# Kernel tuning notes

Hardware: AMD Instinct MI355X
Metric: run time of the kernel (lower is better)

The kernel has to match this reference:

```python
import jax, jax.numpy as jnp
import numpy as np

EPS = 1e-5  # torch BatchNorm default eps
SLOPE = 0.2  # LeakyReLU negative slope


def bn_apply(h, p):
    # p: (4, C) stacked [gamma, beta, running_mean, running_var]; h channel-last
    g, b, m, v = p[0], p[1], p[2], p[3]
    return (h - m) * (g * jax.lax.rsqrt(v + EPS)) + b


def graph_feature(x, k):
    # x: (B, N, C) -> (B, N, k, 2C) = concat(neighbor - center, center)
    inner = jnp.einsum('bnc,bmc->bnm', x, x)
    sq = jnp.sum(x * x, axis=-1)
    # negative squared pairwise distance (B, N, N)
    pd = 2.0 * inner - sq[:, :, None] - sq[:, None, :]
    idx = jax.lax.top_k(pd, k)[1]  # (B, N, k)
    nbr = jax.vmap(lambda xb, ib: xb[ib])(x, idx)  # (B, N, k, C) gather
    ctr = jnp.broadcast_to(x[:, :, None, :], nbr.shape)
    return jnp.concatenate([nbr - ctr, ctr], axis=-1)


def edge_block(h, w, bnp, k):
    # h: (B, N, C); w: (O, 2C) 1x1 conv weight; returns (B, N, O) after max over k
    f = graph_feature(h, k)
    z = jnp.einsum('bnkc,oc->bnko', f, w)
    z = jax.nn.leaky_relu(bn_apply(z, bnp), SLOPE)
    return jnp.max(z, axis=2)


def setup_inputs() -> dict:
    key = jax.random.key(0)
    ks = jax.random.split(key, 10)
    B, N, K = 16, 1024, 20
    emb, ncls = 1024, 40

    def bnp(c):
        return jnp.stack([jnp.ones(c), jnp.zeros(c), jnp.zeros(c), jnp.ones(c)])

    s = 0.05
    return {
        'x': jax.random.normal(ks[0], (B, 3, N), dtype=jnp.float32),
        'w1': jax.random.normal(ks[1], (64, 6), dtype=jnp.float32) * s,
        'bn1': bnp(64),
        'w2': jax.random.normal(ks[2], (64, 128), dtype=jnp.float32) * s,
        'bn2': bnp(64),
        'w3': jax.random.normal(ks[3], (128, 128), dtype=jnp.float32) * s,
        'bn3': bnp(128),
        'w4': jax.random.normal(ks[4], (256, 256), dtype=jnp.float32) * s,
        'bn4': bnp(256),
        'w5': jax.random.normal(ks[5], (emb, 512), dtype=jnp.float32) * s,
        'bn5': bnp(emb),
        'wl1': jax.random.normal(ks[6], (512, 2 * emb), dtype=jnp.float32) * s,
        'bn6': bnp(512),
        'wl2': jax.random.normal(ks[7], (256, 512), dtype=jnp.float32) * s,
        'bn7': bnp(256),
        'wl3': jax.random.normal(ks[8], (ncls, 256), dtype=jnp.float32) * s,
        'bl3': jax.random.normal(ks[9], (ncls,), dtype=jnp.float32) * s,
        'k': K,
    }


def reference(x, w1, bn1, w2, bn2, w3, bn3, w4, bn4, w5, bn5,
              wl1, bn6, wl2, bn7, wl3, bl3, k):
    # x: (B, 3, N) -> logits (B, num_classes); eval-mode BN, dropout = identity
    h0 = jnp.transpose(x, (0, 2, 1))  # (B, N, 3)
    x1 = edge_block(h0, w1, bn1, k)   # (B, N, 64)
    x2 = edge_block(x1, w2, bn2, k)   # (B, N, 64)
    x3 = edge_block(x2, w3, bn3, k)   # (B, N, 128)
    x4 = edge_block(x3, w4, bn4, k)   # (B, N, 256)
    h = jnp.concatenate([x1, x2, x3, x4], axis=-1)  # (B, N, 512)
    h = jax.nn.leaky_relu(bn_apply(jnp.einsum('bnc,oc->bno', h, w5), bn5), SLOPE)
    p = jnp.concatenate([jnp.max(h, axis=1), jnp.mean(h, axis=1)], axis=-1)  # (B, 2*emb)
    h = jax.nn.leaky_relu(bn_apply(p @ wl1.T, bn6), SLOPE)
    h = jax.nn.leaky_relu(bn_apply(h @ wl2.T, bn7), SLOPE)
    return h @ wl3.T + bl3
```

## Files before the change

kernel.cpp:

```cpp
#include <hip/hip_runtime.h>

#define BB 16
#define NN 1024
#define KNN 20
#define BNEPS 1e-5f

typedef __attribute__((ext_vector_type(8))) short short8;
typedef __attribute__((ext_vector_type(4))) float f32x4;

__device__ __forceinline__ float4 ld4(const float* p){ return *(const float4*)p; }
__device__ __forceinline__ void fma4(float4& a, float s, float4 w){
  a.x = fmaf(s, w.x, a.x); a.y = fmaf(s, w.y, a.y);
  a.z = fmaf(s, w.z, a.z); a.w = fmaf(s, w.w, a.w);
}
__device__ __forceinline__ void max4(float4& a, float4 v){
  a.x = fmaxf(a.x, v.x); a.y = fmaxf(a.y, v.y);
  a.z = fmaxf(a.z, v.z); a.w = fmaxf(a.w, v.w);
}
__device__ __forceinline__ unsigned short f2bf(float f){
  unsigned int u = __float_as_uint(f);
  u = (u + 0x7FFF + ((u >> 16) & 1)) >> 16;
  return (unsigned short)u;
}
__device__ __forceinline__ float bf2f(unsigned short u){
  return __uint_as_float(((unsigned int)u) << 16);
}
__device__ __forceinline__ f32x4 mfma16(short8 a, short8 b, f32x4 c){
  return __builtin_amdgcn_mfma_f32_16x16x32_bf16(a, b, c, 0, 0, 0);
}

__device__ __forceinline__ void top3_build(const float* rp, int kmr,
                                           float& a0, float& a1, float& a2,
                                           int& i0, int& i1, int& i2){
  a0 = -1e30f; a1 = -1e30f; a2 = -1e30f; i0 = 0; i1 = 0; i2 = 0;
#pragma unroll
  for (int r = 0; r < 4; r++){
    float4 t = ld4(rp + r*4);
    float tv[4] = {t.x, t.y, t.z, t.w};
#pragma unroll
    for (int q = 0; q < 4; q++){
      int e = r*4 + q;
      float v = ((kmr >> e) & 1) ? -1e30f : tv[q];
      bool b0 = v > a0, b1 = v > a1, b2 = v > a2;
      a2 = b1 ? a1 : (b2 ? v : a2); i2 = b1 ? i1 : (b2 ? e : i2);
      a1 = b0 ? a0 : (b1 ? v : a1); i1 = b0 ? i0 : (b1 ? e : i1);
      a0 = b0 ? v  : a0;            i0 = b0 ? e : i0;
    }
  }
}

__global__ __launch_bounds__(256) void k_transpose(const float* __restrict__ x, float* __restrict__ xt,
                                                   unsigned short* __restrict__ hlo,
                                                   float* __restrict__ sq){
  int i = blockIdx.x*256 + threadIdx.x;
  if (i >= BB*NN) return;
  int b = i >> 10, n = i & 1023;
  const float* xb = x + (size_t)b*3*NN;
  float4 v;
  v.x = xb[0*NN+n]; v.y = xb[1*NN+n]; v.z = xb[2*NN+n]; v.w = 0.f;
  ((float4*)xt)[i] = v;
  unsigned short hx = f2bf(v.x), hy = f2bf(v.y), hz = f2bf(v.z);
  float rx = v.x - bf2f(hx), ry = v.y - bf2f(hy), rz = v.z - bf2f(hz);
  unsigned short lx = f2bf(rx), ly = f2bf(ry), lz = f2bf(rz);
  float ex = bf2f(hx)+bf2f(lx), ey = bf2f(hy)+bf2f(ly), ez = bf2f(hz)+bf2f(lz);
  sq[i] = ex*ex + ey*ey + ez*ez;
  ushort4 h4 = {hx, hy, hz, 0};
  ushort4 l4 = {lx, ly, lz, 0};
  ushort4 z4 = {0, 0, 0, 0};
  unsigned short* pa = hlo + (size_t)i*512 + 256;
  unsigned short* pb = hlo + (size_t)i*512 + 288;
  *(ushort4*)(pa+0) = h4; *(ushort4*)(pa+4) = l4; *(ushort4*)(pa+8) = h4;
  *(ushort4*)(pb+0) = h4; *(ushort4*)(pb+4) = h4; *(ushort4*)(pb+8) = l4;
#pragma unroll
  for (int s = 12; s < 32; s += 4){ *(ushort4*)(pa+s) = z4; *(ushort4*)(pb+s) = z4; }
}

__device__ __forceinline__ void prep_w_dev(int i, const float* w, const float* bnp,
                                           float* wlT, float* dT, float* bias, int Cin, int Cpad, int Cout){
  if (i >= Cpad*Cout) return;
  int c = i / Cout, o = i - c*Cout;
  float s = bnp[o] * rsqrtf(bnp[3*Cout+o] + BNEPS);
  float wl = (c < Cin) ? w[(size_t)o*2*Cin + c] : 0.f;
  float wr = (c < Cin) ? w[(size_t)o*2*Cin + Cin + c] : 0.f;
  wlT[i] = wl * s;
  dT[i]  = (wr - wl) * s;
  if (c == 0) bias[o] = bnp[Cout+o] - bnp[2*Cout+o]*s;
}
__device__ __forceinline__ void prep_wbf_dev(int i, const float* w, const float* bnp,
                                             unsigned short* wlB, unsigned short* dB, float* bias,
                                             int Cin, int Cout){
  if (i >= Cin*Cout) return;
  int o = i / Cin, c = i - o*Cin;
  float s = bnp[o] * rsqrtf(bnp[3*Cout+o] + BNEPS);
  float wl = w[(size_t)o*2*Cin + c] * s;
  float wr = w[(size_t)o*2*Cin + Cin + c] * s;
  wlB[i] = f2bf(wl);
  dB[i]  = f2bf(wr - wl);
  if (c == 0) bias[o] = bnp[Cout+o] - bnp[2*Cout+o]*s;
}

__global__ __launch_bounds__(256) void k_prep_all(const float* __restrict__ w1, const float* __restrict__ bn1,
                                                  const float* __restrict__ w2, const float* __restrict__ bn2,
                                                  const float* __restrict__ w3, const float* __restrict__ bn3,
                                                  const float* __restrict__ w4, const float* __restrict__ bn4,
                                                  const float* __restrict__ w5, const float* __restrict__ bn5,
                                                  float* __restrict__ wlT1, float* __restrict__ dT1, float* __restrict__ bias1,
                                                  unsigned short* __restrict__ wlB2, unsigned short* __restrict__ dB2, float* __restrict__ bias2,
                                                  unsigned short* __restrict__ wlB3, unsigned short* __restrict__ dB3, float* __restrict__ bias3,
                                                  unsigned short* __restrict__ wlB4, unsigned short* __restrict__ dB4, float* __restrict__ bias4,
                                                  unsigned short* __restrict__ w5b, float* __restrict__ b5){
  int bid = blockIdx.x, t = threadIdx.x;
  if (bid < 1){
    prep_w_dev(t, w1, bn1, wlT1, dT1, bias1, 3, 4, 64);
  } else if (bid < 17){
    prep_wbf_dev((bid-1)*256 + t, w2, bn2, wlB2, dB2, bias2, 64, 64);
  } else if (bid < 49){
    prep_wbf_dev((bid-17)*256 + t, w3, bn3, wlB3, dB3, bias3, 64, 128);
  } else if (bid < 177){
    prep_wbf_dev((bid-49)*256 + t, w4, bn4, wlB4, dB4, bias4, 128, 256);
  } else {
    int i = (bid-177)*256 + t;
    int o = i >> 9, c = i & 511;
    float s = bn5[o] * rsqrtf(bn5[3*1024+o] + BNEPS);
    w5b[i] = f2bf(w5[(size_t)o*512 + c] * s);
    if (c == 0) b5[o] = bn5[1024+o] - bn5[2*1024+o]*s;
  }
}

template<int CC>
__global__ __launch_bounds__(256) void k_sqb(const unsigned short* __restrict__ hb,
                                             const unsigned short* __restrict__ hlo,
                                             float* __restrict__ sq){
  int i = blockIdx.x*256 + threadIdx.x;
  if (i >= BB*NN) return;
  const unsigned short* ph = hb  + (size_t)i*512;
  const unsigned short* pl = hlo + (size_t)i*512;
  float s = 0.f;
#pragma unroll
  for (int c = 0; c < CC; c += 4){
    ushort4 a = *(const ushort4*)(ph + c);
    ushort4 b = *(const ushort4*)(pl + c);
    float v0 = bf2f(a.x)+bf2f(b.x), v1 = bf2f(a.y)+bf2f(b.y);
    float v2 = bf2f(a.z)+bf2f(b.z), v3 = bf2f(a.w)+bf2f(b.w);
    s += v0*v0 + v1*v1 + v2*v2 + v3*v3;
  }
  sq[i] = s;
}

template<int CC>
__global__ __launch_bounds__(256) void k_pdm(const unsigned short* __restrict__ hbi,
                                             const unsigned short* __restrict__ hlo,
                                             const float* __restrict__ sq,
                                             float* __restrict__ pd){
  __shared__ char sm[20480];
  char* As = sm; char* Bs = sm + 10240;
  const int tid = threadIdx.x, lane = tid & 63, w = tid >> 6;
  const int l15 = lane & 15, quad = lane >> 4;
  const int bid = blockIdx.x;
  const int xcd = bid & 7, j = bid >> 3;
  const int b = xcd + ((j >> 6) << 3);
  const int rt = (j >> 3) & 7, ct = j & 7;
  const size_t ar0 = (size_t)b*NN + rt*128;
  const size_t br0 = (size_t)b*NN + ct*128;
  const int colb = ct*128;

  f32x4 acc[2][8];
  f32x4 zero = {0.f,0.f,0.f,0.f};
#pragma unroll
  for (int i = 0; i < 2; i++)
#pragma unroll
    for (int j2 = 0; j2 < 8; j2++) acc[i][j2] = zero;

  for (int k0 = 0; k0 < 3*CC; k0 += 32){
    int seg = k0 / CC, off = k0 - seg*CC;
    const unsigned short* Ap = (seg == 1) ? hlo : hbi;
    const unsigned short* Bp = (seg == 2) ? hlo : hbi;
#pragma unroll
    for (int i = 0; i < 2; i++){
      int e = tid + i*256;
      int r = e >> 2, sg = e & 3;
      *(float4*)(As + r*80 + sg*16) = *(const float4*)(Ap + (ar0+r)*512 + off + sg*8);
      *(float4*)(Bs + r*80 + sg*16) = *(const float4*)(Bp + (br0+r)*512 + off + sg*8);
    }
    __syncthreads();
    short8 af0 = *(short8*)(As + (w*32 + l15)*80 + quad*16);
    short8 af1 = *(short8*)(As + (w*32 + 16 + l15)*80 + quad*16);
#pragma unroll
    for (int ns = 0; ns < 8; ns++){
      short8 bf = *(short8*)(Bs + (ns*16 + l15)*80 + quad*16);
      acc[0][ns] = mfma16(af0, bf, acc[0][ns]);
      acc[1][ns] = mfma16(af1, bf, acc[1][ns]);
    }
    __syncthreads();
  }

  float* L = (float*)sm;
#pragma unroll
  for (int p = 0; p < 4; p++){
    const int ms = p >> 1, nh = p & 1;
    __syncthreads();
#pragma unroll
    for (int ns = 0; ns < 4; ns++){
      f32x4 a = acc[ms][nh*4 + ns];
      float sqv = sq[br0 + (nh*4+ns)*16 + l15];
#pragma unroll
      for (int r = 0; r < 4; r++)
        L[(w*16 + quad*4 + r)*68 + ns*16 + l15] = 2.f*a[r] - sqv;
    }
    __syncthreads();
#pragma unroll
    for (int k = 0; k < 4; k++){
      int e = tid + k*256;
      int lr = e >> 4, c4 = (e & 15)*4;
      int grow = (int)ar0 + (lr >> 4)*32 + ms*16 + (lr & 15);
      *(float4*)(pd + (size_t)grow*NN + colb + nh*64 + c4) = *(float4*)(L + lr*68 + c4);
    }
  }
}

__global__ __launch_bounds__(256) void k_pdm1(const unsigned short* __restrict__ hlo,
                                              const float* __restrict__ sq,
                                              float* __restrict__ pd){
  __shared__ char sm[20480];
  char* As = sm; char* Bs = sm + 10240;
  const int tid = threadIdx.x, lane = tid & 63, w = tid >> 6;
  const int l15 = lane & 15, quad = lane >> 4;
  const int bid = blockIdx.x;
  const int xcd = bid & 7, j = bid >> 3;
  const int b = xcd + ((j >> 6) << 3);
  const int rt = (j >> 3) & 7, ct = j & 7;
  const size_t ar0 = (size_t)b*NN + rt*128;
  const size_t br0 = (size_t)b*NN + ct*128;
  const int colb = ct*128;

#pragma unroll
  for (int i = 0; i < 2; i++){
    int e = tid + i*256;
    int r = e >> 2, sg = e & 3;
    *(float4*)(As + r*80 + sg*16) = *(const float4*)(hlo + (ar0+r)*512 + 256 + sg*8);
    *(float4*)(Bs + r*80 + sg*16) = *(const float4*)(hlo + (br0+r)*512 + 288 + sg*8);
  }
  __syncthreads();

  f32x4 acc[2][8];
  f32x4 zero = {0.f,0.f,0.f,0.f};
#pragma unroll
  for (int i = 0; i < 2; i++)
#pragma unroll
    for (int j2 = 0; j2 < 8; j2++) acc[i][j2] = zero;

  short8 af0 = *(short8*)(As + (w*32 + l15)*80 + quad*16);
  short8 af1 = *(short8*)(As + (w*32 + 16 + l15)*80 + quad*16);
#pragma unroll
  for (int ns = 0; ns < 8; ns++){
    short8 bf = *(short8*)(Bs + (ns*16 + l15)*80 + quad*16);
    acc[0][ns] = mfma16(af0, bf, acc[0][ns]);
    acc[1][ns] = mfma16(af1, bf, acc[1][ns]);
  }

  float* L = (float*)sm;
#pragma unroll
  for (int p = 0; p < 4; p++){
    const int ms = p >> 1, nh = p & 1;
    __syncthreads();
#pragma unroll
    for (int ns = 0; ns < 4; ns++){
      f32x4 a = acc[ms][nh*4 + ns];
      float sqv = sq[br0 + (nh*4+ns)*16 + l15];
#pragma unroll
      for (int r = 0; r < 4; r++)
        L[(w*16 + quad*4 + r)*68 + ns*16 + l15] = 2.f*a[r] - sqv;
    }
    __syncthreads();
#pragma unroll
    for (int k = 0; k < 4; k++){
      int e = tid + k*256;
      int lr = e >> 4, c4 = (e & 15)*4;
      int grow = (int)ar0 + (lr >> 4)*32 + ms*16 + (lr & 15);
      *(float4*)(pd + (size_t)grow*NN + colb + nh*64 + c4) = *(float4*)(L + lr*68 + c4);
    }
  }
}

__global__ __launch_bounds__(256) void k_topk(const float* __restrict__ pd, int* __restrict__ idxOut){
  int w = threadIdx.x >> 6, lane = threadIdx.x & 63;
  const int bid = blockIdx.x;
  const int xcd = bid & 7, j = bid >> 3;
  const int b = xcd + ((j >> 7) << 3);
  const int local = j & 127;
  int bn0 = (b*128 + local)*8 + w*2;
  const float* row0 = pd + (size_t)bn0*NN + lane*16;
  const float* row1 = row0 + NN;

  float c0v[2], c1v[2], c2v[2];
  int   c0i[2], c1i[2], c2i[2];
  int   km[2] = {0, 0};
  top3_build(row0, 0, c0v[0], c1v[0], c2v[0], c0i[0], c1i[0], c2i[0]);
  top3_build(row1, 0, c0v[1], c1v[1], c2v[1], c0i[1], c1i[1], c2i[1]);

  int* out0 = idxOut + (size_t)bn0*KNN;
  int* out1 = out0 + KNN;
  for (int it = 0; it < KNN; it++){
    float g0 = c0v[0], g1 = c0v[1];
#pragma unroll
    for (int s = 1; s < 64; s <<= 1){
      g0 = fmaxf(g0, __shfl_xor(g0, s));
      g1 = fmaxf(g1, __shfl_xor(g1, s));
    }
    int o0 = __ffsll(__ballot(c0v[0] == g0)) - 1;
    int o1 = __ffsll(__ballot(c0v[1] == g1)) - 1;
    bool u0 = (lane == o0), u1 = (lane == o1);
    if (u0) out0[it] = lane*16 + c0i[0];
    if (u1) out1[it] = lane*16 + c0i[1];
    km[0] |= u0 ? (1 << c0i[0]) : 0;
    km[1] |= u1 ? (1 << c0i[1]) : 0;
    c0v[0] = u0 ? c1v[0] : c0v[0];  c0i[0] = u0 ? c1i[0] : c0i[0];
    c1v[0] = u0 ? c2v[0] : c1v[0];  c1i[0] = u0 ? c2i[0] : c1i[0];
    c2v[0] = u0 ? -1e30f : c2v[0];
    c0v[1] = u1 ? c1v[1] : c0v[1];  c0i[1] = u1 ? c1i[1] : c0i[1];
    c1v[1] = u1 ? c2v[1] : c1v[1];  c1i[1] = u1 ? c2i[1] : c1i[1];
    c2v[1] = u1 ? -1e30f : c2v[1];
    if (it < KNN-1){
      bool rp0 = (c0v[0] == -1e30f) && (km[0] != 0xFFFF);
      bool rp1 = (c0v[1] == -1e30f) && (km[1] != 0xFFFF);
      if (__ballot(rp0 || rp1)){
        if (rp0) top3_build(row0, km[0], c0v[0], c1v[0], c2v[0], c0i[0], c1i[0], c2i[0]);
        if (rp1) top3_build(row1, km[1], c0v[1], c1v[1], c2v[1], c0i[1], c1i[1], c2i[1]);
      }
    }
  }
}

__global__ __launch_bounds__(256) void k_uv1(const float* __restrict__ xt,
                                             const float* __restrict__ wlT, const float* __restrict__ dT,
                                             float* __restrict__ Z){
  int t = blockIdx.x*256 + threadIdx.x;
  int n = t >> 5, q = t & 31;
  float4 xv = ld4(xt + (size_t)n*4);
  const float* wp = (q < 16) ? (wlT + q*4) : (dT + (q-16)*4);
  float4 a = make_float4(0.f,0.f,0.f,0.f);
  fma4(a, xv.x, ld4(wp + 0*64));
  fma4(a, xv.y, ld4(wp + 1*64));
  fma4(a, xv.z, ld4(wp + 2*64));
  fma4(a, xv.w, ld4(wp + 3*64));
  *(float4*)(Z + (size_t)n*128 + q*4) = a;
}

template<int K>
__global__ __launch_bounds__(256) void k_uv(const unsigned short* __restrict__ hbi,
                                            const unsigned short* __restrict__ wB,
                                            float* __restrict__ Z, int ldz){
  __shared__ char sm[20480];
  char* As = sm; char* Bs = sm + 10240;
  const int tid = threadIdx.x, lane = tid & 63, w = tid >> 6;
  const int l15 = lane & 15, quad = lane >> 4;
  const int n0 = blockIdx.y*128, r0 = blockIdx.x*128;

  f32x4 acc[2][8];
  f32x4 zero = {0.f,0.f,0.f,0.f};
#pragma unroll
  for (int i = 0; i < 2; i++)
#pragma unroll
    for (int j = 0; j < 8; j++) acc[i][j] = zero;

  for (int k0 = 0; k0 < K; k0 += 32){
#pragma unroll
    for (int i = 0; i < 2; i++){
      int e = tid + i*256;
      int r = e >> 2, sg = e & 3;
      *(float4*)(As + r*80 + sg*16) = *(const float4*)(hbi + ((size_t)(r0+r))*512 + k0 + sg*8);
      *(float4*)(Bs + r*80 + sg*16) = *(const float4*)(wB  + ((size_t)(n0+r))*K   + k0 + sg*8);
    }
    __syncthreads();
    short8 af0 = *(short8*)(As + (w*32 + l15)*80 + quad*16);
    short8 af1 = *(short8*)(As + (w*32 + 16 + l15)*80 + quad*16);
#pragma unroll
    for (int ns = 0; ns < 8; ns++){
      short8 bf = *(short8*)(Bs + (ns*16 + l15)*80 + quad*16);
      acc[0][ns] = mfma16(af0, bf, acc[0][ns]);
      acc[1][ns] = mfma16(af1, bf, acc[1][ns]);
    }
    __syncthreads();
  }

#pragma unroll
  for (int ms = 0; ms < 2; ms++){
#pragma unroll
    for (int ns = 0; ns < 8; ns++){
      f32x4 a = acc[ms][ns];
      int row = r0 + w*32 + ms*16 + quad*4;
      int col = n0 + ns*16 + l15;
#pragma unroll
      for (int r = 0; r < 4; r++)
        Z[(size_t)(row+r)*ldz + col] = a[r];
    }
  }
}

template<int COUT, int P, bool WLO>
__global__ __launch_bounds__(256) void k_gmax(const float* __restrict__ Z,
                                              const float* __restrict__ bias,
                                              const int* __restrict__ knn_idx,
                                              unsigned short* __restrict__ hbo,
                                              unsigned short* __restrict__ hloo){
  constexpr int QPP = COUT/4;
  __shared__ int idxS[P*KNN];
  const int tid = threadIdx.x;
  const int p0 = blockIdx.x * P;
  for (int t = tid; t < P*KNN; t += 256) idxS[t] = knn_idx[(size_t)p0*KNN + t];
  __syncthreads();

  const int p = tid / QPP, q = tid - p*QPP;
  const int base = p0 & ~1023;
  const int ldz = 2*COUT;
  const float* Zq = Z + q*4;

  float4 m = make_float4(-1e30f,-1e30f,-1e30f,-1e30f);
#pragma unroll
  for (int j = 0; j < KNN; j++){
    int mr = idxS[p*KNN + j];
    max4(m, ld4(Zq + (size_t)(base + mr)*ldz));
  }
  float4 ctr = ld4(Z + (size_t)(p0+p)*ldz + COUT + q*4);
  float4 bs  = ld4(bias + q*4);
  float4 y;
  y.x = m.x + ctr.x + bs.x; y.x = fmaxf(y.x, 0.2f*y.x);
  y.y = m.y + ctr.y + bs.y; y.y = fmaxf(y.y, 0.2f*y.y);
  y.z = m.z + ctr.z + bs.z; y.z = fmaxf(y.z, 0.2f*y.z);
  y.w = m.w + ctr.w + bs.w; y.w = fmaxf(y.w, 0.2f*y.w);

  size_t pi = (size_t)(p0 + p);
  ushort4 hv; hv.x = f2bf(y.x); hv.y = f2bf(y.y); hv.z = f2bf(y.z); hv.w = f2bf(y.w);
  *(ushort4*)(hbo + pi*512 + q*4) = hv;
  if (WLO){
    ushort4 lv;
    lv.x = f2bf(y.x - bf2f(hv.x)); lv.y = f2bf(y.y - bf2f(hv.y));
    lv.z = f2bf(y.z - bf2f(hv.z)); lv.w = f2bf(y.w - bf2f(hv.w));
    *(ushort4*)(hloo + pi*512 + q*4) = lv;
  }
}

__global__ __launch_bounds__(256) void k_conv5m(const unsigned short* __restrict__ hb,
                                                const unsigned short* __restrict__ w5b,
                                                const float* __restrict__ b5,
                                                float* __restrict__ pmax, float* __restrict__ psum){
  __shared__ char sm[20480 + 4096];
  char* As = sm; char* Bs = sm + 10240;
  float* red = (float*)(sm + 20480);
  const int tid = threadIdx.x, lane = tid & 63, w = tid >> 6;
  const int l15 = lane & 15, quad = lane >> 4;
  const int n0 = blockIdx.y*128, r0 = blockIdx.x*128;

  f32x4 acc[2][8];
  f32x4 zero = {0.f,0.f,0.f,0.f};
#pragma unroll
  for (int i = 0; i < 2; i++)
#pragma unroll
    for (int j = 0; j < 8; j++) acc[i][j] = zero;

  for (int k0 = 0; k0 < 512; k0 += 32){
#pragma unroll
    for (int i = 0; i < 2; i++){
      int e = tid + i*256;
      int r = e >> 2, sg = e & 3;
      *(float4*)(As + r*80 + sg*16) = *(const float4*)(hb  + ((size_t)(r0+r))*512 + k0 + sg*8);
      *(float4*)(Bs + r*80 + sg*16) = *(const float4*)(w5b + ((size_t)(n0+r))*512 + k0 + sg*8);
    }
    __syncthreads();
    short8 af0 = *(short8*)(As + (w*32 + l15)*80 + quad*16);
    short8 af1 = *(short8*)(As + (w*32 + 16 + l15)*80 + quad*16);
#pragma unroll
    for (int ns = 0; ns < 8; ns++){
      short8 bf = *(short8*)(Bs + (ns*16 + l15)*80 + quad*16);
      acc[0][ns] = mfma16(af0, bf, acc[0][ns]);
      acc[1][ns] = mfma16(af1, bf, acc[1][ns]);
    }
    __syncthreads();
  }

#pragma unroll
  for (int ns = 0; ns < 8; ns++){
    float bv = b5[n0 + ns*16 + l15];
    float mx = -1e30f, sum = 0.f;
#pragma unroll
    for (int ms = 0; ms < 2; ms++){
      float* a = (float*)&acc[ms][ns];
#pragma unroll
      for (int r = 0; r < 4; r++){
        float v = a[r] + bv; v = fmaxf(v, 0.2f*v);
        mx = fmaxf(mx, v); sum += v;
      }
    }
    for (int s = 16; s < 64; s <<= 1){
      mx = fmaxf(mx, __shfl_xor(mx, s));
      sum += __shfl_xor(sum, s);
    }
    if (quad == 0){ red[(w*8 + ns)*16 + l15] = mx; red[512 + (w*8 + ns)*16 + l15] = sum; }
  }
  __syncthreads();
  if (tid < 128){
    int ns = tid >> 4, ci = tid & 15;
    float mx = -1e30f, sum = 0.f;
#pragma unroll
    for (int w2 = 0; w2 < 4; w2++){
      mx = fmaxf(mx, red[(w2*8 + ns)*16 + ci]);
      sum += red[512 + (w2*8 + ns)*16 + ci];
    }
    pmax[(size_t)blockIdx.x*1024 + n0 + tid] = mx;
    psum[(size_t)blockIdx.x*1024 + n0 + tid] = sum;
  }
}

__global__ __launch_bounds__(256) void k_fc1(const float* __restrict__ pmax, const float* __restrict__ psum,
                                             const float* __restrict__ wl1, const float* __restrict__ bn6,
                                             float* __restrict__ h1){
  __shared__ float pS[2048];
  const int b = blockIdx.y, t = threadIdx.x;
  for (int f = t; f < 512; f += 256){
    float4 r;
    if (f < 256){
      r = ld4(pmax + (size_t)(b*8)*1024 + f*4);
#pragma unroll
      for (int ch = 1; ch < 8; ch++) max4(r, ld4(pmax + (size_t)(b*8+ch)*1024 + f*4));
    } else {
      int o = (f-256)*4;
      r = ld4(psum + (size_t)(b*8)*1024 + o);
#pragma unroll
      for (int ch = 1; ch < 8; ch++){
        float4 s = ld4(psum + (size_t)(b*8+ch)*1024 + o);
        r.x += s.x; r.y += s.y; r.z += s.z; r.w += s.w;
      }
      r.x *= (1.f/1024.f); r.y *= (1.f/1024.f); r.z *= (1.f/1024.f); r.w *= (1.f/1024.f);
    }
    ((float4*)pS)[f] = r;
  }
  __syncthreads();
  const int ol = t >> 4, ch = t & 15;
  const int o = blockIdx.x*16 + ol;
  const float* wr = wl1 + (size_t)o*2048;
  float acc = 0.f;
#pragma unroll
  for (int j = 0; j < 32; j++){
    int c = ch*4 + j*64;
    float4 wv = ld4(wr + c);
    acc += pS[c]*wv.x + pS[c+1]*wv.y + pS[c+2]*wv.z + pS[c+3]*wv.w;
  }
#pragma unroll
  for (int s = 1; s < 16; s <<= 1) acc += __shfl_xor(acc, s);
  if (ch == 0){
    float s = bn6[o] * rsqrtf(bn6[3*512+o] + BNEPS);
    float y = (acc - bn6[2*512+o])*s + bn6[512+o];
    h1[(size_t)b*512 + o] = fmaxf(y, 0.2f*y);
  }
}

__global__ __launch_bounds__(256) void k_fc2(const float* __restrict__ h1,
                                             const float* __restrict__ wl2, const float* __restrict__ bn7,
                                             float* __restrict__ h2){
  __shared__ float hS[512];
  const int b = blockIdx.y, t = threadIdx.x;
  if (t < 128) ((float4*)hS)[t] = ((const float4*)(h1 + (size_t)b*512))[t];
  __syncthreads();
  const int ol = t >> 4, ch = t & 15;
  const int o = blockIdx.x*16 + ol;
  const float* wr = wl2 + (size_t)o*512;
  float acc = 0.f;
#pragma unroll
  for (int j = 0; j < 8; j++){
    int c = ch*4 + j*64;
    float4 wv = ld4(wr + c);
    acc += hS[c]*wv.x + hS[c+1]*wv.y + hS[c+2]*wv.z + hS[c+3]*wv.w;
  }
#pragma unroll
  for (int s = 1; s < 16; s <<= 1) acc += __shfl_xor(acc, s);
  if (ch == 0){
    float s = bn7[o] * rsqrtf(bn7[3*256+o] + BNEPS);
    float y = (acc - bn7[2*256+o])*s + bn7[256+o];
    h2[(size_t)b*256 + o] = fmaxf(y, 0.2f*y);
  }
}

__global__ __launch_bounds__(64) void k_fc3(const float* __restrict__ h2,
                                            const float* __restrict__ wl3, const float* __restrict__ bl3,
                                            float* __restrict__ out){
  const int o = blockIdx.x, b = blockIdx.y, lane = threadIdx.x;
  float4 wv = ld4(wl3 + (size_t)o*256 + lane*4);
  float4 hv = ld4(h2 + (size_t)b*256 + lane*4);
  float acc = hv.x*wv.x + hv.y*wv.y + hv.z*wv.z + hv.w*wv.w;
#pragma unroll
  for (int s = 1; s < 64; s <<= 1) acc += __shfl_xor(acc, s);
  if (lane == 0) out[(size_t)b*40 + o] = acc + bl3[o];
}

extern "C" void kernel_launch(void* const* d_in, const int* in_sizes, int n_in,
                              void* d_out, int out_size, void* d_ws, size_t ws_size,
                              hipStream_t stream) {
  (void)in_sizes; (void)n_in; (void)out_size; (void)ws_size;
  const float* x   = (const float*)d_in[0];
  const float* w1  = (const float*)d_in[1];
  const float* bn1 = (const float*)d_in[2];
  const float* w2  = (const float*)d_in[3];
  const float* bn2 = (const float*)d_in[4];
  const float* w3  = (const float*)d_in[5];
  const float* bn3 = (const float*)d_in[6];
  const float* w4  = (const float*)d_in[7];
  const float* bn4 = (const float*)d_in[8];
  const float* w5  = (const float*)d_in[9];
  const float* bn5 = (const float*)d_in[10];
  const float* wl1 = (const float*)d_in[11];
  const float* bn6 = (const float*)d_in[12];
  const float* wl2 = (const float*)d_in[13];
  const float* bn7 = (const float*)d_in[14];
  const float* wl3 = (const float*)d_in[15];
  const float* bl3 = (const float*)d_in[16];
  float* out = (float*)d_out;

  float* ws    = (float*)d_ws;
  float* xt    = ws;
  float* sqb   = xt + 65536;
  int*   idxb  = (int*)(sqb + 16384);
  float* pd    = (float*)(idxb + 327680);
  unsigned short* hlo = (unsigned short*)(pd + 16777216);
  float* wlT1  = (float*)(hlo + 8388608);
  float* dT1   = wlT1 + 256;
  float* bias1 = dT1 + 256;
  float* bias2 = bias1 + 64;
  float* bias3 = bias2 + 64;
  float* bias4 = bias3 + 128;
  float* b5    = bias4 + 256;
  float* pmax  = b5 + 1024;
  float* psum  = pmax + 131072;
  float* pool  = psum + 131072;
  float* h1b   = pool + 32768;
  float* h2b   = h1b + 8192;
  unsigned short* hb   = (unsigned short*)(h2b + 4096);
  unsigned short* wlB2 = hb + (size_t)16384*512;
  unsigned short* dB2  = wlB2 + 4096;
  unsigned short* wlB3 = dB2 + 4096;
  unsigned short* dB3  = wlB3 + 8192;
  unsigned short* wlB4 = dB3 + 8192;
  unsigned short* dB4  = wlB4 + 32768;
  unsigned short* w5b  = dB4 + 32768;
  float* Z = pd;

  k_transpose<<<64, 256, 0, stream>>>(x, xt, hlo, sqb);
  k_prep_all<<<2225, 256, 0, stream>>>(w1, bn1, w2, bn2, w3, bn3, w4, bn4, w5, bn5,
                                       wlT1, dT1, bias1, wlB2, dB2, bias2,
                                       wlB3, dB3, bias3, wlB4, dB4, bias4, w5b, b5);

  k_pdm1<<<1024, 256, 0, stream>>>(hlo, sqb, pd);
  k_topk<<<2048, 256, 0, stream>>>(pd, idxb);
  k_uv1<<<2048, 256, 0, stream>>>(xt, wlT1, dT1, Z);
  k_gmax<64,16,true><<<1024, 256, 0, stream>>>(Z, bias1, idxb, hb, hlo);

  k_sqb<64><<<64, 256, 0, stream>>>(hb, hlo, sqb);
  k_pdm<64><<<1024, 256, 0, stream>>>(hb, hlo, sqb, pd);
  k_topk<<<2048, 256, 0, stream>>>(pd, idxb);
  k_uv<64><<<dim3(128,1), 256, 0, stream>>>(hb, wlB2, Z, 128);
  k_gmax<64,16,true><<<1024, 256, 0, stream>>>(Z, bias2, idxb, hb + 64, hlo + 64);

  k_sqb<64><<<64, 256, 0, stream>>>(hb + 64, hlo + 64, sqb);
  k_pdm<64><<<1024, 256, 0, stream>>>(hb + 64, hlo + 64, sqb, pd);
  k_topk<<<2048, 256, 0, stream>>>(pd, idxb);
  k_uv<64><<<dim3(128,2), 256, 0, stream>>>(hb + 64, wlB3, Z, 256);
  k_gmax<128,8,true><<<2048, 256, 0, stream>>>(Z, bias3, idxb, hb + 128, hlo + 128);

  k_sqb<128><<<64, 256, 0, stream>>>(hb + 128, hlo + 128, sqb);
  k_pdm<128><<<1024, 256, 0, stream>>>(hb + 128, hlo + 128, sqb, pd);
  k_topk<<<2048, 256, 0, stream>>>(pd, idxb);
  k_uv<128><<<dim3(128,4), 256, 0, stream>>>(hb + 128, wlB4, Z, 512);
  k_gmax<256,4,false><<<4096, 256, 0, stream>>>(Z, bias4, idxb, hb + 256, nullptr);

  k_conv5m<<<dim3(128,8), 256, 0, stream>>>(hb, w5b, b5, pmax, psum);
  k_fc1<<<dim3(32,16), 256, 0, stream>>>(pmax, psum, wl1, bn6, h1b);
  k_fc2<<<dim3(16,16), 256, 0, stream>>>(h1b, wl2, bn7, h2b);
  k_fc3<<<dim3(40,16), 64, 0, stream>>>(h2b, wl3, bl3, out);
}
```

Measured before the change: 446.9 us.

## Fuse pairwise-distance GEMM with top-k selection using shared-memory distance rows

Merges the distance-matrix kernel and the top-k kernel into one. Each block computes a 16-row stripe of negative squared distances against all 1024 points with MFMA, holds the stripe in LDS (about 64KB), and runs the wave-level top-k directly from it. This removes the write and re-read of the full B×N×N fp32 distance matrix in global memory and two kernel launches per layer. In exchange, B operands are read straight from global memory with no LDS tiling, so B data is reloaded per 16-row stripe, and the large LDS footprint reduces occupancy.

```diff
diff --git a/kernel.cpp b/kernel.cpp
--- a/kernel.cpp
+++ b/kernel.cpp
@@ -147,185 +147,166 @@
   sq[i] = s;
 }
 
+#define PDSTR 1028
 template<int CC>
-__global__ __launch_bounds__(256) void k_pdm(const unsigned short* __restrict__ hbi,
-                                             const unsigned short* __restrict__ hlo,
-                                             const float* __restrict__ sq,
-                                             float* __restrict__ pd){
-  __shared__ char sm[20480];
-  char* As = sm; char* Bs = sm + 10240;
+__global__ __launch_bounds__(256) void k_pdtopk(const unsigned short* __restrict__ hbi,
+                                                const unsigned short* __restrict__ hloi,
+                                                const float* __restrict__ sq,
+                                                int* __restrict__ idxOut){
+  __shared__ float pdrow[16*PDSTR];
   const int tid = threadIdx.x, lane = tid & 63, w = tid >> 6;
   const int l15 = lane & 15, quad = lane >> 4;
   const int bid = blockIdx.x;
   const int xcd = bid & 7, j = bid >> 3;
   const int b = xcd + ((j >> 6) << 3);
-  const int rt = (j >> 3) & 7, ct = j & 7;
-  const size_t ar0 = (size_t)b*NN + rt*128;
-  const size_t br0 = (size_t)b*NN + ct*128;
-  const int colb = ct*128;
-
-  f32x4 acc[2][8];
+  const int stripe = j & 63;
+  const size_t ar0 = (size_t)b*NN + stripe*16;
+  const size_t brow = (size_t)b*NN;
+
+  constexpr int KF = CC/32;
+  short8 afr[3*KF];
+#pragma unroll
+  for (int s = 0; s < 3; s++){
+    const unsigned short* Ap = (s == 1) ? hloi : hbi;
+#pragma unroll
+    for (int k = 0; k < KF; k++)
+      afr[s*KF + k] = *(const short8*)(Ap + (ar0 + l15)*512 + k*32 + quad*8);
+  }
+
   f32x4 zero = {0.f,0.f,0.f,0.f};
 #pragma unroll
-  for (int i = 0; i < 2; i++)
-#pragma unroll
-    for (int j2 = 0; j2 < 8; j2++) acc[i][j2] = zero;
-
-  for (int k0 = 0; k0 < 3*CC; k0 += 32){
-    int seg = k0 / CC, off = k0 - seg*CC;
-    const unsigned short* Ap = (seg == 1) ? hlo : hbi;
-    const unsigned short* Bp = (seg == 2) ? hlo : hbi;
-#pragma unroll
-    for (int i = 0; i < 2; i++){
-      int e = tid + i*256;
-      int r = e >> 2, sg = e & 3;
-      *(float4*)(As + r*80 + sg*16) = *(const float4*)(Ap + (ar0+r)*512 + off + sg*8);
-      *(float4*)(Bs + r*80 + sg*16) = *(const float4*)(Bp + (br0+r)*512 + off + sg*8);
-    }
-    __syncthreads();
-    short8 af0 = *(short8*)(As + (w*32 + l15)*80 + quad*16);
-    short8 af1 = *(short8*)(As + (w*32 + 16 + l15)*80 + quad*16);
-#pragma unroll
-    for (int ns = 0; ns < 8; ns++){
-      short8 bf = *(short8*)(Bs + (ns*16 + l15)*80 + quad*16);
-      acc[0][ns] = mfma16(af0, bf, acc[0][ns]);
-      acc[1][ns] = mfma16(af1, bf, acc[1][ns]);
-    }
-    __syncthreads();
-  }
-
-  float* L = (float*)sm;
-#pragma unroll
-  for (int p = 0; p < 4; p++){
-    const int ms = p >> 1, nh = p & 1;
-    __syncthreads();
-#pragma unroll
-    for (int ns = 0; ns < 4; ns++){
-      f32x4 a = acc[ms][nh*4 + ns];
-      float sqv = sq[br0 + (nh*4+ns)*16 + l15];
-#pragma unroll
-      for (int r = 0; r < 4; r++)
-        L[(w*16 + quad*4 + r)*68 + ns*16 + l15] = 2.f*a[r] - sqv;
-    }
-    __syncthreads();
-#pragma unroll
-    for (int k = 0; k < 4; k++){
-      int e = tid + k*256;
-      int lr = e >> 4, c4 = (e & 15)*4;
-      int grow = (int)ar0 + (lr >> 4)*32 + ms*16 + (lr & 15);
-      *(float4*)(pd + (size_t)grow*NN + colb + nh*64 + c4) = *(float4*)(L + lr*68 + c4);
-    }
-  }
-}
-
-__global__ __launch_bounds__(256) void k_pdm1(const unsigned short* __restrict__ hlo,
-                                              const float* __restrict__ sq,
-                                              float* __restrict__ pd){
-  __shared__ char sm[20480];
-  char* As = sm; char* Bs = sm + 10240;
+  for (int c = 0; c < 16; c++){
+    const int colb = (w*16 + c)*16;
+    f32x4 acc = zero;
+#pragma unroll
+    for (int s = 0; s < 3; s++){
+      const unsigned short* Bp = (s == 2) ? hloi : hbi;
+#pragma unroll
+      for (int k = 0; k < KF; k++){
+        short8 bf = *(const short8*)(Bp + (brow + colb + l15)*512 + k*32 + quad*8);
+        acc = mfma16(afr[s*KF + k], bf, acc);
+      }
+    }
+    float sqv = sq[b*NN + colb + l15];
+#pragma unroll
+    for (int r = 0; r < 4; r++)
+      pdrow[(quad*4 + r)*PDSTR + colb + l15] = 2.f*acc[r] - sqv;
+  }
+  __syncthreads();
+
+  for (int p = 0; p < 2; p++){
+    const int rl0 = p*8 + w*2;
+    const float* row0 = pdrow + rl0*PDSTR + lane*16;
+    const float* row1 = row0 + PDSTR;
+
+    float c0v[2], c1v[2], c2v[2];
+    int   c0i[2], c1i[2], c2i[2];
+    int   km[2] = {0, 0};
+    top3_build(row0, 0, c0v[0], c1v[0], c2v[0], c0i[0], c1i[0], c2i[0]);
+    top3_build(row1, 0, c0v[1], c1v[1], c2v[1], c0i[1], c1i[1], c2i[1]);
+
+    int* out0 = idxOut + (ar0 + rl0)*KNN;
+    int* out1 = out0 + KNN;
+    for (int it = 0; it < KNN; it++){
+      float g0 = c0v[0], g1 = c0v[1];
+#pragma unroll
+      for (int s = 1; s < 64; s <<= 1){
+        g0 = fmaxf(g0, __shfl_xor(g0, s));
+        g1 = fmaxf(g1, __shfl_xor(g1, s));
+      }
+      int o0 = __ffsll(__ballot(c0v[0] == g0)) - 1;
+      int o1 = __ffsll(__ballot(c0v[1] == g1)) - 1;
+      bool u0 = (lane == o0), u1 = (lane == o1);
+      if (u0) out0[it] = lane*16 + c0i[0];
+      if (u1) out1[it] = lane*16 + c0i[1];
+      km[0] |= u0 ? (1 << c0i[0]) : 0;
+      km[1] |= u1 ? (1 << c0i[1]) : 0;
+      c0v[0] = u0 ? c1v[0] : c0v[0];  c0i[0] = u0 ? c1i[0] : c0i[0];
+      c1v[0] = u0 ? c2v[0] : c1v[0];  c1i[0] = u0 ? c2i[0] : c1i[0];
+      c2v[0] = u0 ? -1e30f : c2v[0];
+      c0v[1] = u1 ? c1v[1] : c0v[1];  c0i[1] = u1 ? c1i[1] : c0i[1];
+      c1v[1] = u1 ? c2v[1] : c1v[1];  c1i[1] = u1 ? c2i[1] : c1i[1];
+      c2v[1] = u1 ? -1e30f : c2v[1];
+      if (it < KNN-1){
+        bool rp0 = (c0v[0] == -1e30f) && (km[0] != 0xFFFF);
+        bool rp1 = (c0v[1] == -1e30f) && (km[1] != 0xFFFF);
+        if (__ballot(rp0 || rp1)){
+          if (rp0) top3_build(row0, km[0], c0v[0], c1v[0], c2v[0], c0i[0], c1i[0], c2i[0]);
+          if (rp1) top3_build(row1, km[1], c0v[1], c1v[1], c2v[1], c0i[1], c1i[1], c2i[1]);
+        }
+      }
+    }
+  }
+}
+
+__global__ __launch_bounds__(256) void k_pdtopk1(const unsigned short* __restrict__ hloi,
+                                                 const float* __restrict__ sq,
+                                                 int* __restrict__ idxOut){
+  __shared__ float pdrow[16*PDSTR];
   const int tid = threadIdx.x, lane = tid & 63, w = tid >> 6;
   const int l15 = lane & 15, quad = lane >> 4;
   const int bid = blockIdx.x;
   const int xcd = bid & 7, j = bid >> 3;
   const int b = xcd + ((j >> 6) << 3);
-  const int rt = (j >> 3) & 7, ct = j & 7;
-  const size_t ar0 = (size_t)b*NN + rt*128;
-  const size_t br0 = (size_t)b*NN + ct*128;
-  const int colb = ct*128;
-
-#pragma unroll
-  for (int i = 0; i < 2; i++){
-    int e = tid + i*256;
-    int r = e >> 2, sg = e & 3;
-    *(float4*)(As + r*80 + sg*16) = *(const float4*)(hlo + (ar0+r)*512 + 256 + sg*8);
-    *(float4*)(Bs + r*80 + sg*16) = *(const float4*)(hlo + (br0+r)*512 + 288 + sg*8);
+  const int stripe = j & 63;
+  const size_t ar0 = (size_t)b*NN + stripe*16;
+  const size_t brow = (size_t)b*NN;
+
+  short8 af = *(const short8*)(hloi + (ar0 + l15)*512 + 256 + quad*8);
+
+  f32x4 zero = {0.f,0.f,0.f,0.f};
+#pragma unroll
+  for (int c = 0; c < 16; c++){
+    const int colb = (w*16 + c)*16;
+    short8 bf = *(const short8*)(hloi + (brow + colb + l15)*512 + 288 + quad*8);
+    f32x4 acc = mfma16(af, bf, zero);
+    float sqv = sq[b*NN + colb + l15];
+#pragma unroll
+    for (int r = 0; r < 4; r++)
+      pdrow[(quad*4 + r)*PDSTR + colb + l15] = 2.f*acc[r] - sqv;
   }
   __syncthreads();
 
-  f32x4 acc[2][8];
-  f32x4 zero = {0.f,0.f,0.f,0.f};
-#pragma unroll
-  for (int i = 0; i < 2; i++)
-#pragma unroll
-    for (int j2 = 0; j2 < 8; j2++) acc[i][j2] = zero;
-
-  short8 af0 = *(short8*)(As + (w*32 + l15)*80 + quad*16);
-  short8 af1 = *(short8*)(As + (w*32 + 16 + l15)*80 + quad*16);
-#pragma unroll
-  for (int ns = 0; ns < 8; ns++){
-    short8 bf = *(short8*)(Bs + (ns*16 + l15)*80 + quad*16);
-    acc[0][ns] = mfma16(af0, bf, acc[0][ns]);
-    acc[1][ns] = mfma16(af1, bf, acc[1][ns]);
-  }
-
-  float* L = (float*)sm;
-#pragma unroll
-  for (int p = 0; p < 4; p++){
-    const int ms = p >> 1, nh = p & 1;
-    __syncthreads();
-#pragma unroll
-    for (int ns = 0; ns < 4; ns++){
-      f32x4 a = acc[ms][nh*4 + ns];
-      float sqv = sq[br0 + (nh*4+ns)*16 + l15];
-#pragma unroll
-      for (int r = 0; r < 4; r++)
-        L[(w*16 + quad*4 + r)*68 + ns*16 + l15] = 2.f*a[r] - sqv;
-    }
-    __syncthreads();
-#pragma unroll
-    for (int k = 0; k < 4; k++){
-      int e = tid + k*256;
-      int lr = e >> 4, c4 = (e & 15)*4;
-      int grow = (int)ar0 + (lr >> 4)*32 + ms*16 + (lr & 15);
-      *(float4*)(pd + (size_t)grow*NN + colb + nh*64 + c4) = *(float4*)(L + lr*68 + c4);
-    }
-  }
-}
-
-__global__ __launch_bounds__(256) void k_topk(const float* __restrict__ pd, int* __restrict__ idxOut){
-  int w = threadIdx.x >> 6, lane = threadIdx.x & 63;
-  const int bid = blockIdx.x;
-  const int xcd = bid & 7, j = bid >> 3;
-  const int b = xcd + ((j >> 7) << 3);
-  const int local = j & 127;
-  int bn0 = (b*128 + local)*8 + w*2;
-  const float* row0 = pd + (size_t)bn0*NN + lane*16;
-  const float* row1 = row0 + NN;
-
-  float c0v[2], c1v[2], c2v[2];
-  int   c0i[2], c1i[2], c2i[2];
-  int   km[2] = {0, 0};
-  top3_build(row0, 0, c0v[0], c1v[0], c2v[0], c0i[0], c1i[0], c2i[0]);
-  top3_build(row1, 0, c0v[1], c1v[1], c2v[1], c0i[1], c1i[1], c2i[1]);
-
-  int* out0 = idxOut + (size_t)bn0*KNN;
-  int* out1 = out0 + KNN;
-  for (int it = 0; it < KNN; it++){
-    float g0 = c0v[0], g1 = c0v[1];
-#pragma unroll
-    for (int s = 1; s < 64; s <<= 1){
-      g0 = fmaxf(g0, __shfl_xor(g0, s));
-      g1 = fmaxf(g1, __shfl_xor(g1, s));
-    }
-    int o0 = __ffsll(__ballot(c0v[0] == g0)) - 1;
-    int o1 = __ffsll(__ballot(c0v[1] == g1)) - 1;
-    bool u0 = (lane == o0), u1 = (lane == o1);
-    if (u0) out0[it] = lane*16 + c0i[0];
-    if (u1) out1[it] = lane*16 + c0i[1];
-    km[0] |= u0 ? (1 << c0i[0]) : 0;
-    km[1] |= u1 ? (1 << c0i[1]) : 0;
-    c0v[0] = u0 ? c1v[0] : c0v[0];  c0i[0] = u0 ? c1i[0] : c0i[0];
-    c1v[0] = u0 ? c2v[0] : c1v[0];  c1i[0] = u0 ? c2i[0] : c1i[0];
-    c2v[0] = u0 ? -1e30f : c2v[0];
-    c0v[1] = u1 ? c1v[1] : c0v[1];  c0i[1] = u1 ? c1i[1] : c0i[1];
-    c1v[1] = u1 ? c2v[1] : c1v[1];  c1i[1] = u1 ? c2i[1] : c1i[1];
-    c2v[1] = u1 ? -1e30f : c2v[1];
-    if (it < KNN-1){
-      bool rp0 = (c0v[0] == -1e30f) && (km[0] != 0xFFFF);
-      bool rp1 = (c0v[1] == -1e30f) && (km[1] != 0xFFFF);
-      if (__ballot(rp0 || rp1)){
-        if (rp0) top3_build(row0, km[0], c0v[0], c1v[0], c2v[0], c0i[0], c1i[0], c2i[0]);
-        if (rp1) top3_build(row1, km[1], c0v[1], c1v[1], c2v[1], c0i[1], c1i[1], c2i[1]);
+  for (int p = 0; p < 2; p++){
+    const int rl0 = p*8 + w*2;
+    const float* row0 = pdrow + rl0*PDSTR + lane*16;
+    const float* row1 = row0 + PDSTR;
+
+    float c0v[2], c1v[2], c2v[2];
+    int   c0i[2], c1i[2], c2i[2];
+    int   km[2] = {0, 0};
+    top3_build(row0, 0, c0v[0], c1v[0], c2v[0], c0i[0], c1i[0], c2i[0]);
+    top3_build(row1, 0, c0v[1], c1v[1], c2v[1], c0i[1], c1i[1], c2i[1]);
+
+    int* out0 = idxOut + (ar0 + rl0)*KNN;
+    int* out1 = out0 + KNN;
+    for (int it = 0; it < KNN; it++){
+      float g0 = c0v[0], g1 = c0v[1];
+#pragma unroll
+      for (int s = 1; s < 64; s <<= 1){
+        g0 = fmaxf(g0, __shfl_xor(g0, s));
+        g1 = fmaxf(g1, __shfl_xor(g1, s));
+      }
+      int o0 = __ffsll(__ballot(c0v[0] == g0)) - 1;
+      int o1 = __ffsll(__ballot(c0v[1] == g1)) - 1;
+      bool u0 = (lane == o0), u1 = (lane == o1);
+      if (u0) out0[it] = lane*16 + c0i[0];
+      if (u1) out1[it] = lane*16 + c0i[1];
+      km[0] |= u0 ? (1 << c0i[0]) : 0;
+      km[1] |= u1 ? (1 << c0i[1]) : 0;
+      c0v[0] = u0 ? c1v[0] : c0v[0];  c0i[0] = u0 ? c1i[0] : c0i[0];
+      c1v[0] = u0 ? c2v[0] : c1v[0];  c1i[0] = u0 ? c2i[0] : c1i[0];
+      c2v[0] = u0 ? -1e30f : c2v[0];
+      c0v[1] = u1 ? c1v[1] : c0v[1];  c0i[1] = u1 ? c1i[1] : c0i[1];
+      c1v[1] = u1 ? c2v[1] : c1v[1];  c1i[1] = u1 ? c2i[1] : c1i[1];
+      c2v[1] = u1 ? -1e30f : c2v[1];
+      if (it < KNN-1){
+        bool rp0 = (c0v[0] == -1e30f) && (km[0] != 0xFFFF);
+        bool rp1 = (c0v[1] == -1e30f) && (km[1] != 0xFFFF);
+        if (__ballot(rp0 || rp1)){
+          if (rp0) top3_build(row0, km[0], c0v[0], c1v[0], c2v[0], c0i[0], c1i[0], c2i[0]);
+          if (rp1) top3_build(row1, km[1], c0v[1], c1v[1], c2v[1], c0i[1], c1i[1], c2i[1]);
+        }
       }
     }
   }
@@ -648,26 +629,22 @@
                                        wlT1, dT1, bias1, wlB2, dB2, bias2,
                                        wlB3, dB3, bias3, wlB4, dB4, bias4, w5b, b5);
 
-  k_pdm1<<<1024, 256, 0, stream>>>(hlo, sqb, pd);
-  k_topk<<<2048, 256, 0, stream>>>(pd, idxb);
+  k_pdtopk1<<<1024, 256, 0, stream>>>(hlo, sqb, idxb);
   k_uv1<<<2048, 256, 0, stream>>>(xt, wlT1, dT1, Z);
   k_gmax<64,16,true><<<1024, 256, 0, stream>>>(Z, bias1, idxb, hb, hlo);
 
   k_sqb<64><<<64, 256, 0, stream>>>(hb, hlo, sqb);
-  k_pdm<64><<<1024, 256, 0, stream>>>(hb, hlo, sqb, pd);
-  k_topk<<<2048, 256, 0, stream>>>(pd, idxb);
+  k_pdtopk<64><<<1024, 256, 0, stream>>>(hb, hlo, sqb, idxb);
   k_uv<64><<<dim3(128,1), 256, 0, stream>>>(hb, wlB2, Z, 128);
   k_gmax<64,16,true><<<1024, 256, 0, stream>>>(Z, bias2, idxb, hb + 64, hlo + 64);
 
   k_sqb<64><<<64, 256, 0, stream>>>(hb + 64, hlo + 64, sqb);
-  k_pdm<64><<<1024, 256, 0, stream>>>(hb + 64, hlo + 64, sqb, pd);
-  k_topk<<<2048, 256, 0, stream>>>(pd, idxb);
+  k_pdtopk<64><<<1024, 256, 0, stream>>>(hb + 64, hlo + 64, sqb, idxb);
   k_uv<64><<<dim3(128,2), 256, 0, stream>>>(hb + 64, wlB3, Z, 256);
   k_gmax<128,8,true><<<2048, 256, 0, stream>>>(Z, bias3, idxb, hb + 128, hlo + 128);
 
   k_sqb<128><<<64, 256, 0, stream>>>(hb + 128, hlo + 128, sqb);
-  k_pdm<128><<<1024, 256, 0, stream>>>(hb + 128, hlo + 128, sqb, pd);
-  k_topk<<<2048, 256, 0, stream>>>(pd, idxb);
+  k_pdtopk<128><<<1024, 256, 0, stream>>>(hb + 128, hlo + 128, sqb, idxb);
   k_uv<128><<<dim3(128,4), 256, 0, stream>>>(hb + 128, wlB4, Z, 512);
   k_gmax<256,4,false><<<4096, 256, 0, stream>>>(Z, bias4, idxb, hb + 256, nullptr);
 
```

New measurement: 498.4 us. +11.5%, slower.

## Fuse squared-norm computation into gather-max and remap blocks for XCD locality

Applied to the files above, without the earlier changes.

The separate k_sqb kernel is removed. Each point's squared norm is now computed inside k_gmax from the hi/lo bf16 outputs, using a lane shuffle reduction, which drops three launches and a re-read of the features. Block indices in k_uv1, k_uv and k_gmax are also permuted so that consecutive blocks on the same XCD handle the same batch, which should improve L2 locality for the gathered Z rows. The shuffle reduction assumes that the QPP lanes of one point are contiguous within a wavefront.

```diff
diff --git a/kernel.cpp b/kernel.cpp
--- a/kernel.cpp
+++ b/kernel.cpp
@@ -128,26 +128,6 @@
 }
 
 template<int CC>
-__global__ __launch_bounds__(256) void k_sqb(const unsigned short* __restrict__ hb,
-                                             const unsigned short* __restrict__ hlo,
-                                             float* __restrict__ sq){
-  int i = blockIdx.x*256 + threadIdx.x;
-  if (i >= BB*NN) return;
-  const unsigned short* ph = hb  + (size_t)i*512;
-  const unsigned short* pl = hlo + (size_t)i*512;
-  float s = 0.f;
-#pragma unroll
-  for (int c = 0; c < CC; c += 4){
-    ushort4 a = *(const ushort4*)(ph + c);
-    ushort4 b = *(const ushort4*)(pl + c);
-    float v0 = bf2f(a.x)+bf2f(b.x), v1 = bf2f(a.y)+bf2f(b.y);
-    float v2 = bf2f(a.z)+bf2f(b.z), v3 = bf2f(a.w)+bf2f(b.w);
-    s += v0*v0 + v1*v1 + v2*v2 + v3*v3;
-  }
-  sq[i] = s;
-}
-
-template<int CC>
 __global__ __launch_bounds__(256) void k_pdm(const unsigned short* __restrict__ hbi,
                                              const unsigned short* __restrict__ hlo,
                                              const float* __restrict__ sq,
@@ -334,7 +314,9 @@
 __global__ __launch_bounds__(256) void k_uv1(const float* __restrict__ xt,
                                              const float* __restrict__ wlT, const float* __restrict__ dT,
                                              float* __restrict__ Z){
-  int t = blockIdx.x*256 + threadIdx.x;
+  const int bid = blockIdx.x;
+  const int pb = ((bid >> 10) << 10) | ((bid & 7) << 7) | ((bid >> 3) & 127);
+  int t = pb*256 + threadIdx.x;
   int n = t >> 5, q = t & 31;
   float4 xv = ld4(xt + (size_t)n*4);
   const float* wp = (q < 16) ? (wlT + q*4) : (dT + (q-16)*4);
@@ -354,7 +336,9 @@
   char* As = sm; char* Bs = sm + 10240;
   const int tid = threadIdx.x, lane = tid & 63, w = tid >> 6;
   const int l15 = lane & 15, quad = lane >> 4;
-  const int n0 = blockIdx.y*128, r0 = blockIdx.x*128;
+  const int bx = blockIdx.x;
+  const int t = ((bx & 7) << 3) | ((bx >> 3) & 7) | (bx & 64);
+  const int n0 = blockIdx.y*128, r0 = t*128;
 
   f32x4 acc[2][8];
   f32x4 zero = {0.f,0.f,0.f,0.f};
@@ -402,11 +386,16 @@
                                               const float* __restrict__ bias,
                                               const int* __restrict__ knn_idx,
                                               unsigned short* __restrict__ hbo,
-                                              unsigned short* __restrict__ hloo){
+                                              unsigned short* __restrict__ hloo,
+                                              float* __restrict__ sqo){
   constexpr int QPP = COUT/4;
+  constexpr int BPB = 1024/P;
+  constexpr int SHF = (P == 16) ? 6 : (P == 8) ? 7 : 8;
   __shared__ int idxS[P*KNN];
   const int tid = threadIdx.x;
-  const int p0 = blockIdx.x * P;
+  const int bid = blockIdx.x;
+  const int pb = ((bid >> (SHF+3)) << (SHF+3)) | ((bid & 7) << SHF) | ((bid >> 3) & (BPB-1));
+  const int p0 = pb * P;
   for (int t = tid; t < P*KNN; t += 256) idxS[t] = knn_idx[(size_t)p0*KNN + t];
   __syncthreads();
 
@@ -437,6 +426,12 @@
     lv.x = f2bf(y.x - bf2f(hv.x)); lv.y = f2bf(y.y - bf2f(hv.y));
     lv.z = f2bf(y.z - bf2f(hv.z)); lv.w = f2bf(y.w - bf2f(hv.w));
     *(ushort4*)(hloo + pi*512 + q*4) = lv;
+    float ex = bf2f(hv.x)+bf2f(lv.x), ey = bf2f(hv.y)+bf2f(lv.y);
+    float ez = bf2f(hv.z)+bf2f(lv.z), ew = bf2f(hv.w)+bf2f(lv.w);
+    float s4 = ex*ex + ey*ey + ez*ez + ew*ew;
+#pragma unroll
+    for (int sh = 1; sh < QPP; sh <<= 1) s4 += __shfl_xor(s4, sh);
+    if (q == 0) sqo[pi] = s4;
   }
 }
 
@@ -651,25 +646,22 @@
   k_pdm1<<<1024, 256, 0, stream>>>(hlo, sqb, pd);
   k_topk<<<2048, 256, 0, stream>>>(pd, idxb);
   k_uv1<<<2048, 256, 0, stream>>>(xt, wlT1, dT1, Z);
-  k_gmax<64,16,true><<<1024, 256, 0, stream>>>(Z, bias1, idxb, hb, hlo);
-
-  k_sqb<64><<<64, 256, 0, stream>>>(hb, hlo, sqb);
+  k_gmax<64,16,true><<<1024, 256, 0, stream>>>(Z, bias1, idxb, hb, hlo, sqb);
+
   k_pdm<64><<<1024, 256, 0, stream>>>(hb, hlo, sqb, pd);
   k_topk<<<2048, 256, 0, stream>>>(pd, idxb);
   k_uv<64><<<dim3(128,1), 256, 0, stream>>>(hb, wlB2, Z, 128);
-  k_gmax<64,16,true><<<1024, 256, 0, stream>>>(Z, bias2, idxb, hb + 64, hlo + 64);
-
-  k_sqb<64><<<64, 256, 0, stream>>>(hb + 64, hlo + 64, sqb);
+  k_gmax<64,16,true><<<1024, 256, 0, stream>>>(Z, bias2, idxb, hb + 64, hlo + 64, sqb);
+
   k_pdm<64><<<1024, 256, 0, stream>>>(hb + 64, hlo + 64, sqb, pd);
   k_topk<<<2048, 256, 0, stream>>>(pd, idxb);
   k_uv<64><<<dim3(128,2), 256, 0, stream>>>(hb + 64, wlB3, Z, 256);
-  k_gmax<128,8,true><<<2048, 256, 0, stream>>>(Z, bias3, idxb, hb + 128, hlo + 128);
-
-  k_sqb<128><<<64, 256, 0, stream>>>(hb + 128, hlo + 128, sqb);
+  k_gmax<128,8,true><<<2048, 256, 0, stream>>>(Z, bias3, idxb, hb + 128, hlo + 128, sqb);
+
   k_pdm<128><<<1024, 256, 0, stream>>>(hb + 128, hlo + 128, sqb, pd);
   k_topk<<<2048, 256, 0, stream>>>(pd, idxb);
   k_uv<128><<<dim3(128,4), 256, 0, stream>>>(hb + 128, wlB4, Z, 512);
-  k_gmax<256,4,false><<<4096, 256, 0, stream>>>(Z, bias4, idxb, hb + 256, nullptr);
+  k_gmax<256,4,false><<<4096, 256, 0, stream>>>(Z, bias4, idxb, hb + 256, nullptr, nullptr);
 
   k_conv5m<<<dim3(128,8), 256, 0, stream>>>(hb, w5b, b5, pmax, psum);
   k_fc1<<<dim3(32,16), 256, 0, stream>>>(pmax, psum, wl1, bn6, h1b);
```

After: 422.1 us. 1.06x faster.
